# Performance work log

Measured on AMD Instinct MI355X. Metric: run time of the kernel, lower is better.

Reference implementation:

```python
import jax, jax.numpy as jnp
import numpy as np

B, F, D, K, H, W = 8, 16, 256, 3, 64, 64

def setup_inputs() -> dict:
    key = jax.random.key(0)
    k1, k2, k3, k4 = jax.random.split(key, 4)
    return {
        "x": jax.random.normal(k1, (B, D, H, W), dtype=jnp.float32),
        "bank_request": jax.random.normal(k2, (B, F), dtype=jnp.float32),
        "style": jax.random.normal(k3, (B, 1, D, 1, 1), dtype=jnp.float32),
        "bank_weight": jax.random.normal(k4, (F, D, D, K, K), dtype=jnp.float32),
    }

def reference(x, bank_request, style, bank_weight):
    # softmax-weighted filter bank sum -> per-sample kernel (b, o, i, kh, kw)
    w = jax.nn.softmax(bank_request, axis=1)                      # (b, f)
    kernel = jnp.einsum('bf,foihw->boihw', w, bank_weight)
    # style modulation
    kernel = kernel * (1.0 + style)
    # L2 demodulation over (i, kh, kw)
    norm = jax.lax.rsqrt(jnp.sum(kernel * kernel, axis=(2, 3, 4), keepdims=True) + 1e-8)
    kernel = kernel * norm
    # per-sample conv2d, stride 1, SAME padding (odd symmetric kernel)
    def conv_one(xi, ki):
        return jax.lax.conv_general_dilated(
            xi[None], ki, window_strides=(1, 1), padding='SAME',
            dimension_numbers=('NCHW', 'OIHW', 'NCHW'))[0]
    return jax.vmap(conv_one)(x, kernel)
```

## Files before the change

kernel.cpp:

```cpp
#include <hip/hip_runtime.h>
#include <hip/hip_bf16.h>
#include <math.h>

#define BB 8
#define FF 16
#define DD 256
#define HH 64
#define WW 64

typedef short bf16x8 __attribute__((ext_vector_type(8)));
typedef float f32x4 __attribute__((ext_vector_type(4)));

__device__ inline ushort f2bf(float f) {
    union { float f; unsigned u; } v; v.f = f;
    unsigned r = v.u + 0x7FFFu + ((v.u >> 16) & 1u);
    return (ushort)(r >> 16);
}

__global__ __launch_bounds__(256) void cast_x(
    const float* __restrict__ x,
    ushort* __restrict__ xb)
{
    __shared__ ushort ls[64][258];
    const int r = blockIdx.x, b = blockIdx.y, t = threadIdx.x;

    const int c4 = (t & 15) * 4;
    const int ig = t >> 4;
#pragma unroll
    for (int j = 0; j < 16; ++j) {
        const int i = ig * 16 + j;
        const float4 xv = *reinterpret_cast<const float4*>(
            x + (((size_t)(b * DD + i) * HH) + r) * WW + c4);
        ls[c4 + 0][i] = f2bf(xv.x);
        ls[c4 + 1][i] = f2bf(xv.y);
        ls[c4 + 2][i] = f2bf(xv.z);
        ls[c4 + 3][i] = f2bf(xv.w);
    }
    __syncthreads();

    const int i2 = t & 127;
    const int ch = t >> 7;
#pragma unroll
    for (int cl = 0; cl < 32; ++cl) {
        const int c = ch * 32 + cl;
        const unsigned u = (unsigned)ls[c][2 * i2] | ((unsigned)ls[c][2 * i2 + 1] << 16);
        *reinterpret_cast<unsigned*>(xb + (((size_t)(b * HH + r) * WW) + c) * DD + 2 * i2) = u;
    }
}

__global__ __launch_bounds__(256) void prep_filter(
    const float* __restrict__ bank_request,
    const float* __restrict__ style,
    const float* __restrict__ bank_weight,
    ushort* __restrict__ Ak)
{
    const int o = blockIdx.x;
    const int i = threadIdx.x;

    __shared__ float wsm[BB][FF];
    __shared__ float red[4][BB];
    __shared__ float nrm[BB];

    if (i < BB) {
        float v[FF];
        float m = -1e30f;
#pragma unroll
        for (int f = 0; f < FF; ++f) {
            v[f] = bank_request[i * FF + f];
            m = fmaxf(m, v[f]);
        }
        float s = 0.f;
#pragma unroll
        for (int f = 0; f < FF; ++f) { v[f] = __expf(v[f] - m); s += v[f]; }
        const float inv = 1.0f / s;
#pragma unroll
        for (int f = 0; f < FF; ++f) wsm[i][f] = v[f] * inv;
    }
    __syncthreads();

    float acc9[BB][9];
#pragma unroll
    for (int b = 0; b < BB; ++b)
#pragma unroll
        for (int j = 0; j < 9; ++j) acc9[b][j] = 0.f;

    float pre[2][9];
#pragma unroll
    for (int s = 0; s < 2; ++s) {
        const float* p = bank_weight + ((size_t)(s * DD + o) * DD + i) * 9;
#pragma unroll
        for (int j = 0; j < 9; ++j) pre[s][j] = p[j];
    }
#pragma unroll
    for (int f = 0; f < FF; ++f) {
        const int sl = f & 1;
        float cur[9];
#pragma unroll
        for (int j = 0; j < 9; ++j) cur[j] = pre[sl][j];
        if (f + 2 < FF) {
            const float* p = bank_weight + ((size_t)((f + 2) * DD + o) * DD + i) * 9;
#pragma unroll
            for (int j = 0; j < 9; ++j) pre[sl][j] = p[j];
        }
#pragma unroll
        for (int b = 0; b < BB; ++b) {
            const float wf = wsm[b][f];
#pragma unroll
            for (int j = 0; j < 9; ++j) acc9[b][j] = fmaf(wf, cur[j], acc9[b][j]);
        }
    }

    float ss[BB];
#pragma unroll
    for (int b = 0; b < BB; ++b) {
        const float sm = 1.0f + style[b * DD + i];
        float t = 0.f;
#pragma unroll
        for (int j = 0; j < 9; ++j) {
            acc9[b][j] *= sm;
            t = fmaf(acc9[b][j], acc9[b][j], t);
        }
        ss[b] = t;
    }

    const int wave = i >> 6, lane = i & 63;
#pragma unroll
    for (int b = 0; b < BB; ++b) {
        float tv = ss[b];
#pragma unroll
        for (int off = 32; off > 0; off >>= 1) tv += __shfl_down(tv, off, 64);
        if (lane == 0) red[wave][b] = tv;
    }
    __syncthreads();
    if (i < BB)
        nrm[i] = rsqrtf(red[0][i] + red[1][i] + red[2][i] + red[3][i] + 1e-8f);
    __syncthreads();

    const int ib = i >> 3, e = i & 7;
#pragma unroll
    for (int b = 0; b < BB; ++b) {
        const float nb = nrm[b];
#pragma unroll
        for (int j = 0; j < 9; ++j) {
            const size_t idx = ((((size_t)(b * 9 + j) * 32 + ib) * DD) + o) * 8 + e;
            Ak[idx] = f2bf(acc9[b][j] * nb);
        }
    }
}

#define XROWS 4
#define XCELLS 66
#define XCELLB 80
#define XBUF (XROWS * XCELLS * XCELLB)

__global__ __launch_bounds__(512, 4) void conv_mfma(
    const ushort* __restrict__ xb,
    const ushort* __restrict__ Ak,
    float* __restrict__ out)
{
    __shared__ __align__(16) char xs[2 * XBUF];

    const int wg = blockIdx.x;
    const int xcd = wg & 7;
    const int rem = wg >> 3;
    const int rg = rem & 31;
    const int Ghi = rem >> 5;
    const int G = xcd + 8 * Ghi;
    const int ot = G & 1, b = G >> 1;

    const int r0 = rg * 2, o0 = ot * 128;
    const int t = threadIdx.x;
    const int w = t >> 6, l = t & 63;
    const int wm = w & 3;
    const int wn = w >> 2;
    const int lo = l & 15, lhi = l >> 4;

    const ushort* sg_ptr[3];
    int sg_lds[3];
    bool sg_ok[3];
#pragma unroll
    for (int s = 0; s < 3; ++s) {
        const int idx = t + s * 512;
        const bool active = (s < 2) || (t < 32);
        const int row = idx / (XCELLS * 4);
        const int rem2 = idx - row * (XCELLS * 4);
        const int cell = rem2 >> 2;
        const int q = rem2 & 3;
        const int gr = r0 - 1 + row;
        const int gc = cell - 1;
        sg_ok[s] = active && ((unsigned)gr < 64u) && ((unsigned)gc < 64u);
        sg_ptr[s] = xb + (((size_t)(b * HH + (gr & 63)) * WW) + (gc & 63)) * DD + q * 8;
        sg_lds[s] = (row * XCELLS + cell) * XCELLB + q * 16;
    }
    const bool sg_act2 = (t < 32);

    f32x4 acc[2][4];
#pragma unroll
    for (int a = 0; a < 2; ++a)
#pragma unroll
        for (int c = 0; c < 4; ++c)
#pragma unroll
            for (int j = 0; j < 4; ++j) acc[a][c][j] = 0.f;

    const int obase = o0 + wm * 32 + lo;
    const int bLane = lo * XCELLB + lhi * 16;

    bf16x8 vr[3];
    bf16x8 aF[3][2], bF[2][4];

#define LDA(tp, sl, aB)  do {                                                  \
        const ushort* ap_ = (aB) + (size_t)(tp) * 65536;                       \
        aF[sl][0] = *reinterpret_cast<const bf16x8*>(ap_);                     \
        aF[sl][1] = *reinterpret_cast<const bf16x8*>(ap_ + 128);               \
    } while (0)

#define LDB(tp, sl, bufc)  do {                                                \
        const int dr_ = (tp) / 3, dc_ = (tp) % 3;                              \
        const char* bb_ = (bufc) + ((wn + dr_) * XCELLS + dc_) * XCELLB;       \
        bF[sl][0] = *reinterpret_cast<const bf16x8*>(bb_);                     \
        bF[sl][1] = *reinterpret_cast<const bf16x8*>(bb_ + 16 * XCELLB);       \
        bF[sl][2] = *reinterpret_cast<const bf16x8*>(bb_ + 32 * XCELLB);       \
        bF[sl][3] = *reinterpret_cast<const bf16x8*>(bb_ + 48 * XCELLB);       \
    } while (0)

#pragma unroll
    for (int s = 0; s < 3; ++s) {
        if (s < 2 || sg_act2) {
            bf16x8 v = {0, 0, 0, 0, 0, 0, 0, 0};
            if (sg_ok[s]) v = *reinterpret_cast<const bf16x8*>(sg_ptr[s]);
            *reinterpret_cast<bf16x8*>(xs + sg_lds[s]) = v;
        }
    }
    __syncthreads();

    for (int kc = 0; kc < 8; ++kc) {
        const int cur = kc & 1;

        if (kc < 7) {
            const int ioff = (kc + 1) * 32;
#pragma unroll
            for (int s = 0; s < 3; ++s) {
                bf16x8 v = {0, 0, 0, 0, 0, 0, 0, 0};
                if (sg_ok[s]) v = *reinterpret_cast<const bf16x8*>(sg_ptr[s] + ioff);
                vr[s] = v;
            }
        }

        const char* bufc = xs + cur * XBUF + bLane;
        const int ib = kc * 4 + lhi;
        const ushort* aBase = Ak + (((size_t)b * 9 * 32 + ib) * DD + obase) * 8;

        LDA(0, 0, aBase);
        LDA(1, 1, aBase);
        LDB(0, 0, bufc);
#pragma unroll
        for (int tap = 0; tap < 9; ++tap) {
            const int as = tap % 3;
            if (tap + 2 <= 8) LDA(tap + 2, (tap + 2) % 3, aBase);
            if (tap < 8) LDB(tap + 1, (tap + 1) & 1, bufc);
            const int bs = tap & 1;
            __builtin_amdgcn_s_setprio(1);
#pragma unroll
            for (int fm = 0; fm < 2; ++fm)
#pragma unroll
                for (int fn = 0; fn < 4; ++fn)
                    acc[fm][fn] = __builtin_amdgcn_mfma_f32_16x16x32_bf16(
                        aF[as][fm], bF[bs][fn], acc[fm][fn], 0, 0, 0);
            __builtin_amdgcn_s_setprio(0);
        }

        if (kc < 7) {
            char* dstb = xs + (cur ^ 1) * XBUF;
#pragma unroll
            for (int s = 0; s < 3; ++s)
                if (s < 2 || sg_act2)
                    *reinterpret_cast<bf16x8*>(dstb + sg_lds[s]) = vr[s];
        }
        __syncthreads();
    }
#undef LDA
#undef LDB

    const int r_out = r0 + wn;
#pragma unroll
    for (int fm = 0; fm < 2; ++fm) {
#pragma unroll
        for (int fn = 0; fn < 4; ++fn) {
            const int oo = o0 + wm * 32 + fm * 16 + lhi * 4;
            const int cc = fn * 16 + lo;
            float* op = out + (((size_t)(b * DD + oo) * HH) + r_out) * WW + cc;
#pragma unroll
            for (int j = 0; j < 4; ++j) op[(size_t)j * HH * WW] = acc[fm][fn][j];
        }
    }
}

extern "C" void kernel_launch(void* const* d_in, const int* in_sizes, int n_in,
                              void* d_out, int out_size, void* d_ws, size_t ws_size,
                              hipStream_t stream) {
    const float* x            = (const float*)d_in[0];
    const float* bank_request = (const float*)d_in[1];
    const float* style        = (const float*)d_in[2];
    const float* bank_weight  = (const float*)d_in[3];
    float* out = (float*)d_out;

    ushort* Ak = (ushort*)d_ws;
    ushort* xb = Ak + (size_t)8 * 9 * 32 * 256 * 8;

    cast_x<<<dim3(HH, BB), 256, 0, stream>>>(x, xb);
    prep_filter<<<dim3(DD), 256, 0, stream>>>(bank_request, style, bank_weight, Ak);
    conv_mfma<<<dim3(512), 512, 0, stream>>>(xb, Ak, out);
}
```

Baseline: 68.26 us.

## Switch conv to 32x32x16 MFMA with 256-thread blocks and 64x64 wave tiles

Replaces the 16x16x32 bf16 MFMA tiling with 32x32x16 MFMAs, splitting each 32-channel K chunk into two 16-wide substeps. Each workgroup now uses 4 waves instead of 8, each covering a 64x64 output tile, so each wave issues fewer fragment loads per MFMA. The staging loop and the epilogue index mapping are reworked for the new thread count and accumulator layout. Fewer waves per block could reduce latency hiding, and more accumulator registers per wave may lower occupancy.

```diff
diff --git a/kernel.cpp b/kernel.cpp
--- a/kernel.cpp
+++ b/kernel.cpp
@@ -9,7 +9,7 @@
 #define WW 64
 
 typedef short bf16x8 __attribute__((ext_vector_type(8)));
-typedef float f32x4 __attribute__((ext_vector_type(4)));
+typedef float f32x16 __attribute__((ext_vector_type(16)));
 
 __device__ inline ushort f2bf(float f) {
     union { float f; unsigned u; } v; v.f = f;
@@ -153,7 +153,7 @@
 #define XCELLB 80
 #define XBUF (XROWS * XCELLS * XCELLB)
 
-__global__ __launch_bounds__(512, 4) void conv_mfma(
+__global__ __launch_bounds__(256, 2) void conv_mfma(
     const ushort* __restrict__ xb,
     const ushort* __restrict__ Ak,
     float* __restrict__ out)
@@ -171,61 +171,62 @@
     const int r0 = rg * 2, o0 = ot * 128;
     const int t = threadIdx.x;
     const int w = t >> 6, l = t & 63;
-    const int wm = w & 3;
-    const int wn = w >> 2;
-    const int lo = l & 15, lhi = l >> 4;
-
-    const ushort* sg_ptr[3];
-    int sg_lds[3];
-    bool sg_ok[3];
-#pragma unroll
-    for (int s = 0; s < 3; ++s) {
-        const int idx = t + s * 512;
-        const bool active = (s < 2) || (t < 32);
+    const int wm = w >> 1;
+    const int wn = w & 1;
+    const int l31 = l & 31, lhi = l >> 5;
+
+    const ushort* sg_ptr[5];
+    int sg_lds[5];
+    bool sg_ok[5];
+    bool sg_act[5];
+#pragma unroll
+    for (int s = 0; s < 5; ++s) {
+        const int idx = t + s * 256;
+        sg_act[s] = (s < 4) || (t < 32);
         const int row = idx / (XCELLS * 4);
         const int rem2 = idx - row * (XCELLS * 4);
         const int cell = rem2 >> 2;
         const int q = rem2 & 3;
         const int gr = r0 - 1 + row;
         const int gc = cell - 1;
-        sg_ok[s] = active && ((unsigned)gr < 64u) && ((unsigned)gc < 64u);
+        sg_ok[s] = sg_act[s] && ((unsigned)gr < 64u) && ((unsigned)gc < 64u);
         sg_ptr[s] = xb + (((size_t)(b * HH + (gr & 63)) * WW) + (gc & 63)) * DD + q * 8;
         sg_lds[s] = (row * XCELLS + cell) * XCELLB + q * 16;
     }
-    const bool sg_act2 = (t < 32);
-
-    f32x4 acc[2][4];
+
+    f32x16 acc[2][2];
 #pragma unroll
     for (int a = 0; a < 2; ++a)
 #pragma unroll
-        for (int c = 0; c < 4; ++c)
-#pragma unroll
-            for (int j = 0; j < 4; ++j) acc[a][c][j] = 0.f;
-
-    const int obase = o0 + wm * 32 + lo;
-    const int bLane = lo * XCELLB + lhi * 16;
-
-    bf16x8 vr[3];
-    bf16x8 aF[3][2], bF[2][4];
-
-#define LDA(tp, sl, aB)  do {                                                  \
-        const ushort* ap_ = (aB) + (size_t)(tp) * 65536;                       \
+        for (int c = 0; c < 2; ++c)
+#pragma unroll
+            for (int j = 0; j < 16; ++j) acc[a][c][j] = 0.f;
+
+    const int obase = o0 + wm * 64 + l31;
+    const int bLane = l31 * XCELLB + lhi * 16;
+
+    bf16x8 vr[5];
+    bf16x8 aF[3][2], bF[2][2];
+
+#define LDA(stp, sl, aB)  do {                                                 \
+        const int tp_ = (stp) >> 1, ks_ = (stp) & 1;                           \
+        const ushort* ap_ = (aB) + tp_ * 65536 + ks_ * 4096;                   \
         aF[sl][0] = *reinterpret_cast<const bf16x8*>(ap_);                     \
-        aF[sl][1] = *reinterpret_cast<const bf16x8*>(ap_ + 128);               \
+        aF[sl][1] = *reinterpret_cast<const bf16x8*>(ap_ + 256);               \
     } while (0)
 
-#define LDB(tp, sl, bufc)  do {                                                \
-        const int dr_ = (tp) / 3, dc_ = (tp) % 3;                              \
-        const char* bb_ = (bufc) + ((wn + dr_) * XCELLS + dc_) * XCELLB;       \
+#define LDB(stp, sl, bufc)  do {                                               \
+        const int tp_ = (stp) >> 1, ks_ = (stp) & 1;                           \
+        const int dr_ = tp_ / 3, dc_ = tp_ % 3;                                \
+        const char* bb_ = (bufc) + ((wn + dr_) * XCELLS + dc_) * XCELLB        \
+                          + ks_ * 32;                                          \
         bF[sl][0] = *reinterpret_cast<const bf16x8*>(bb_);                     \
-        bF[sl][1] = *reinterpret_cast<const bf16x8*>(bb_ + 16 * XCELLB);       \
-        bF[sl][2] = *reinterpret_cast<const bf16x8*>(bb_ + 32 * XCELLB);       \
-        bF[sl][3] = *reinterpret_cast<const bf16x8*>(bb_ + 48 * XCELLB);       \
+        bF[sl][1] = *reinterpret_cast<const bf16x8*>(bb_ + 32 * XCELLB);       \
     } while (0)
 
 #pragma unroll
-    for (int s = 0; s < 3; ++s) {
-        if (s < 2 || sg_act2) {
+    for (int s = 0; s < 5; ++s) {
+        if (sg_act[s]) {
             bf16x8 v = {0, 0, 0, 0, 0, 0, 0, 0};
             if (sg_ok[s]) v = *reinterpret_cast<const bf16x8*>(sg_ptr[s]);
             *reinterpret_cast<bf16x8*>(xs + sg_lds[s]) = v;
@@ -239,7 +240,7 @@
         if (kc < 7) {
             const int ioff = (kc + 1) * 32;
 #pragma unroll
-            for (int s = 0; s < 3; ++s) {
+            for (int s = 0; s < 5; ++s) {
                 bf16x8 v = {0, 0, 0, 0, 0, 0, 0, 0};
                 if (sg_ok[s]) v = *reinterpret_cast<const bf16x8*>(sg_ptr[s] + ioff);
                 vr[s] = v;
@@ -247,24 +248,28 @@
         }
 
         const char* bufc = xs + cur * XBUF + bLane;
-        const int ib = kc * 4 + lhi;
-        const ushort* aBase = Ak + (((size_t)b * 9 * 32 + ib) * DD + obase) * 8;
-
-        LDA(0, 0, aBase);
-        LDA(1, 1, aBase);
+        const ushort* aBase =
+            Ak + ((((size_t)b * 9 * 32) + kc * 4 + lhi * 1) * DD + obase) * 8
+               + 0;
+        const ushort* aLane =
+            Ak + ((((size_t)b * 9 * 32) + kc * 4 + lhi) * DD + obase) * 8;
+        (void)aBase;
+
+        LDA(0, 0, aLane);
+        LDA(1, 1, aLane);
         LDB(0, 0, bufc);
 #pragma unroll
-        for (int tap = 0; tap < 9; ++tap) {
-            const int as = tap % 3;
-            if (tap + 2 <= 8) LDA(tap + 2, (tap + 2) % 3, aBase);
-            if (tap < 8) LDB(tap + 1, (tap + 1) & 1, bufc);
-            const int bs = tap & 1;
+        for (int stp = 0; stp < 18; ++stp) {
+            const int as = stp % 3;
+            if (stp + 2 < 18) LDA(stp + 2, (stp + 2) % 3, aLane);
+            if (stp + 1 < 18) LDB(stp + 1, (stp + 1) & 1, bufc);
+            const int bs = stp & 1;
             __builtin_amdgcn_s_setprio(1);
 #pragma unroll
             for (int fm = 0; fm < 2; ++fm)
 #pragma unroll
-                for (int fn = 0; fn < 4; ++fn)
-                    acc[fm][fn] = __builtin_amdgcn_mfma_f32_16x16x32_bf16(
+                for (int fn = 0; fn < 2; ++fn)
+                    acc[fm][fn] = __builtin_amdgcn_mfma_f32_32x32x16_bf16(
                         aF[as][fm], bF[bs][fn], acc[fm][fn], 0, 0, 0);
             __builtin_amdgcn_s_setprio(0);
         }
@@ -272,9 +277,8 @@
         if (kc < 7) {
             char* dstb = xs + (cur ^ 1) * XBUF;
 #pragma unroll
-            for (int s = 0; s < 3; ++s)
-                if (s < 2 || sg_act2)
-                    *reinterpret_cast<bf16x8*>(dstb + sg_lds[s]) = vr[s];
+            for (int s = 0; s < 5; ++s)
+                if (sg_act[s]) *reinterpret_cast<bf16x8*>(dstb + sg_lds[s]) = vr[s];
         }
         __syncthreads();
     }
@@ -285,12 +289,15 @@
 #pragma unroll
     for (int fm = 0; fm < 2; ++fm) {
 #pragma unroll
-        for (int fn = 0; fn < 4; ++fn) {
-            const int oo = o0 + wm * 32 + fm * 16 + lhi * 4;
-            const int cc = fn * 16 + lo;
-            float* op = out + (((size_t)(b * DD + oo) * HH) + r_out) * WW + cc;
-#pragma unroll
-            for (int j = 0; j < 4; ++j) op[(size_t)j * HH * WW] = acc[fm][fn][j];
+        for (int fn = 0; fn < 2; ++fn) {
+            const int cc = fn * 32 + l31;
+#pragma unroll
+            for (int reg = 0; reg < 16; ++reg) {
+                const int oo = o0 + wm * 64 + fm * 32
+                             + (reg & 3) + 8 * (reg >> 2) + 4 * lhi;
+                out[(((size_t)(b * DD + oo) * HH) + r_out) * WW + cc] =
+                    acc[fm][fn][reg];
+            }
         }
     }
 }
@@ -309,5 +316,5 @@
 
     cast_x<<<dim3(HH, BB), 256, 0, stream>>>(x, xb);
     prep_filter<<<dim3(DD), 256, 0, stream>>>(bank_request, style, bank_weight, Ak);
-    conv_mfma<<<dim3(512), 512, 0, stream>>>(xb, Ak, out);
-}
+    conv_mfma<<<dim3(512), 256, 0, stream>>>(xb, Ak, out);
+}
```

After: 71.58 us. 4.9% more time.

## Fuse prep kernels and retile conv to one output row per block

Applied to the files above, without the earlier changes.

The x-cast and filter-prep kernels are merged into one launch, with block ranges selecting the role, so one kernel launch and its tail are removed. The conv kernel drops from 512-thread blocks covering two output rows to 256-thread blocks covering one row, doubling the grid and shrinking the LDS halo buffer from 4 to 3 rows. The global prefetch of the next channel chunk moves to mid-tap, behind a sched barrier, to overlap with MFMA work. Per-output halo reuse drops (3 input rows per output row instead of 2), trading extra LDS fill traffic for more blocks and better occupancy.

```diff
diff --git a/kernel.cpp b/kernel.cpp
--- a/kernel.cpp
+++ b/kernel.cpp
@@ -17,50 +17,52 @@
     return (ushort)(r >> 16);
 }
 
-__global__ __launch_bounds__(256) void cast_x(
+__global__ __launch_bounds__(256) void prep_fused(
     const float* __restrict__ x,
-    ushort* __restrict__ xb)
-{
-    __shared__ ushort ls[64][258];
-    const int r = blockIdx.x, b = blockIdx.y, t = threadIdx.x;
-
-    const int c4 = (t & 15) * 4;
-    const int ig = t >> 4;
-#pragma unroll
-    for (int j = 0; j < 16; ++j) {
-        const int i = ig * 16 + j;
-        const float4 xv = *reinterpret_cast<const float4*>(
-            x + (((size_t)(b * DD + i) * HH) + r) * WW + c4);
-        ls[c4 + 0][i] = f2bf(xv.x);
-        ls[c4 + 1][i] = f2bf(xv.y);
-        ls[c4 + 2][i] = f2bf(xv.z);
-        ls[c4 + 3][i] = f2bf(xv.w);
-    }
-    __syncthreads();
-
-    const int i2 = t & 127;
-    const int ch = t >> 7;
-#pragma unroll
-    for (int cl = 0; cl < 32; ++cl) {
-        const int c = ch * 32 + cl;
-        const unsigned u = (unsigned)ls[c][2 * i2] | ((unsigned)ls[c][2 * i2 + 1] << 16);
-        *reinterpret_cast<unsigned*>(xb + (((size_t)(b * HH + r) * WW) + c) * DD + 2 * i2) = u;
-    }
-}
-
-__global__ __launch_bounds__(256) void prep_filter(
     const float* __restrict__ bank_request,
     const float* __restrict__ style,
     const float* __restrict__ bank_weight,
+    ushort* __restrict__ xb,
     ushort* __restrict__ Ak)
 {
-    const int o = blockIdx.x;
-    const int i = threadIdx.x;
-
+    __shared__ ushort ls[64][258];
     __shared__ float wsm[BB][FF];
     __shared__ float red[4][BB];
     __shared__ float nrm[BB];
 
+    const int t = threadIdx.x;
+
+    if (blockIdx.x < 512) {
+        const int r = blockIdx.x & 63, b = blockIdx.x >> 6;
+
+        const int c4 = (t & 15) * 4;
+        const int ig = t >> 4;
+#pragma unroll
+        for (int j = 0; j < 16; ++j) {
+            const int i = ig * 16 + j;
+            const float4 xv = *reinterpret_cast<const float4*>(
+                x + (((size_t)(b * DD + i) * HH) + r) * WW + c4);
+            ls[c4 + 0][i] = f2bf(xv.x);
+            ls[c4 + 1][i] = f2bf(xv.y);
+            ls[c4 + 2][i] = f2bf(xv.z);
+            ls[c4 + 3][i] = f2bf(xv.w);
+        }
+        __syncthreads();
+
+        const int i2 = t & 127;
+        const int ch = t >> 7;
+#pragma unroll
+        for (int cl = 0; cl < 32; ++cl) {
+            const int c = ch * 32 + cl;
+            const unsigned u = (unsigned)ls[c][2 * i2] | ((unsigned)ls[c][2 * i2 + 1] << 16);
+            *reinterpret_cast<unsigned*>(xb + (((size_t)(b * HH + r) * WW) + c) * DD + 2 * i2) = u;
+        }
+        return;
+    }
+
+    const int o = blockIdx.x - 512;
+    const int i = t;
+
     if (i < BB) {
         float v[FF];
         float m = -1e30f;
@@ -114,13 +116,13 @@
 #pragma unroll
     for (int b = 0; b < BB; ++b) {
         const float sm = 1.0f + style[b * DD + i];
-        float t = 0.f;
+        float tv = 0.f;
 #pragma unroll
         for (int j = 0; j < 9; ++j) {
             acc9[b][j] *= sm;
-            t = fmaf(acc9[b][j], acc9[b][j], t);
-        }
-        ss[b] = t;
+            tv = fmaf(acc9[b][j], acc9[b][j], tv);
+        }
+        ss[b] = tv;
     }
 
     const int wave = i >> 6, lane = i & 63;
@@ -148,12 +150,12 @@
     }
 }
 
-#define XROWS 4
+#define XROWS 3
 #define XCELLS 66
 #define XCELLB 80
 #define XBUF (XROWS * XCELLS * XCELLB)
 
-__global__ __launch_bounds__(512, 4) void conv_mfma(
+__global__ __launch_bounds__(256, 4) void conv_mfma(
     const ushort* __restrict__ xb,
     const ushort* __restrict__ Ak,
     float* __restrict__ out)
@@ -163,36 +165,34 @@
     const int wg = blockIdx.x;
     const int xcd = wg & 7;
     const int rem = wg >> 3;
-    const int rg = rem & 31;
-    const int Ghi = rem >> 5;
+    const int r0 = rem & 63;
+    const int Ghi = rem >> 6;
     const int G = xcd + 8 * Ghi;
     const int ot = G & 1, b = G >> 1;
 
-    const int r0 = rg * 2, o0 = ot * 128;
+    const int o0 = ot * 128;
     const int t = threadIdx.x;
     const int w = t >> 6, l = t & 63;
-    const int wm = w & 3;
-    const int wn = w >> 2;
     const int lo = l & 15, lhi = l >> 4;
 
-    const ushort* sg_ptr[3];
-    int sg_lds[3];
-    bool sg_ok[3];
-#pragma unroll
-    for (int s = 0; s < 3; ++s) {
-        const int idx = t + s * 512;
-        const bool active = (s < 2) || (t < 32);
+    const ushort* sg_ptr[4];
+    int sg_lds[4];
+    bool sg_ok[4];
+    bool sg_act[4];
+#pragma unroll
+    for (int s = 0; s < 4; ++s) {
+        const int idx = t + s * 256;
+        sg_act[s] = (s < 3) || (t < 792 - 768);
         const int row = idx / (XCELLS * 4);
         const int rem2 = idx - row * (XCELLS * 4);
         const int cell = rem2 >> 2;
         const int q = rem2 & 3;
         const int gr = r0 - 1 + row;
         const int gc = cell - 1;
-        sg_ok[s] = active && ((unsigned)gr < 64u) && ((unsigned)gc < 64u);
+        sg_ok[s] = sg_act[s] && ((unsigned)gr < 64u) && ((unsigned)gc < 64u);
         sg_ptr[s] = xb + (((size_t)(b * HH + (gr & 63)) * WW) + (gc & 63)) * DD + q * 8;
         sg_lds[s] = (row * XCELLS + cell) * XCELLB + q * 16;
     }
-    const bool sg_act2 = (t < 32);
 
     f32x4 acc[2][4];
 #pragma unroll
@@ -202,10 +202,10 @@
 #pragma unroll
             for (int j = 0; j < 4; ++j) acc[a][c][j] = 0.f;
 
-    const int obase = o0 + wm * 32 + lo;
+    const int obase = o0 + w * 32 + lo;
     const int bLane = lo * XCELLB + lhi * 16;
 
-    bf16x8 vr[3];
+    bf16x8 vr[4];
     bf16x8 aF[3][2], bF[2][4];
 
 #define LDA(tp, sl, aB)  do {                                                  \
@@ -216,7 +216,7 @@
 
 #define LDB(tp, sl, bufc)  do {                                                \
         const int dr_ = (tp) / 3, dc_ = (tp) % 3;                              \
-        const char* bb_ = (bufc) + ((wn + dr_) * XCELLS + dc_) * XCELLB;       \
+        const char* bb_ = (bufc) + (dr_ * XCELLS + dc_) * XCELLB;              \
         bF[sl][0] = *reinterpret_cast<const bf16x8*>(bb_);                     \
         bF[sl][1] = *reinterpret_cast<const bf16x8*>(bb_ + 16 * XCELLB);       \
         bF[sl][2] = *reinterpret_cast<const bf16x8*>(bb_ + 32 * XCELLB);       \
@@ -224,8 +224,8 @@
     } while (0)
 
 #pragma unroll
-    for (int s = 0; s < 3; ++s) {
-        if (s < 2 || sg_act2) {
+    for (int s = 0; s < 4; ++s) {
+        if (sg_act[s]) {
             bf16x8 v = {0, 0, 0, 0, 0, 0, 0, 0};
             if (sg_ok[s]) v = *reinterpret_cast<const bf16x8*>(sg_ptr[s]);
             *reinterpret_cast<bf16x8*>(xs + sg_lds[s]) = v;
@@ -235,28 +235,18 @@
 
     for (int kc = 0; kc < 8; ++kc) {
         const int cur = kc & 1;
-
-        if (kc < 7) {
-            const int ioff = (kc + 1) * 32;
-#pragma unroll
-            for (int s = 0; s < 3; ++s) {
-                bf16x8 v = {0, 0, 0, 0, 0, 0, 0, 0};
-                if (sg_ok[s]) v = *reinterpret_cast<const bf16x8*>(sg_ptr[s] + ioff);
-                vr[s] = v;
-            }
-        }
-
         const char* bufc = xs + cur * XBUF + bLane;
         const int ib = kc * 4 + lhi;
-        const ushort* aBase = Ak + (((size_t)b * 9 * 32 + ib) * DD + obase) * 8;
-
-        LDA(0, 0, aBase);
-        LDA(1, 1, aBase);
+        const ushort* aLane =
+            Ak + ((((size_t)b * 9 * 32) + ib) * DD + obase) * 8;
+
+        LDA(0, 0, aLane);
+        LDA(1, 1, aLane);
         LDB(0, 0, bufc);
 #pragma unroll
         for (int tap = 0; tap < 9; ++tap) {
             const int as = tap % 3;
-            if (tap + 2 <= 8) LDA(tap + 2, (tap + 2) % 3, aBase);
+            if (tap + 2 <= 8) LDA(tap + 2, (tap + 2) % 3, aLane);
             if (tap < 8) LDB(tap + 1, (tap + 1) & 1, bufc);
             const int bs = tap & 1;
             __builtin_amdgcn_s_setprio(1);
@@ -267,28 +257,37 @@
                     acc[fm][fn] = __builtin_amdgcn_mfma_f32_16x16x32_bf16(
                         aF[as][fm], bF[bs][fn], acc[fm][fn], 0, 0, 0);
             __builtin_amdgcn_s_setprio(0);
+
+            if (tap == 4 && kc < 7) {
+                __builtin_amdgcn_sched_barrier(0);
+                const int ioff = (kc + 1) * 32;
+#pragma unroll
+                for (int s = 0; s < 4; ++s) {
+                    bf16x8 v = {0, 0, 0, 0, 0, 0, 0, 0};
+                    if (sg_ok[s]) v = *reinterpret_cast<const bf16x8*>(sg_ptr[s] + ioff);
+                    vr[s] = v;
+                }
+            }
         }
 
         if (kc < 7) {
             char* dstb = xs + (cur ^ 1) * XBUF;
 #pragma unroll
-            for (int s = 0; s < 3; ++s)
-                if (s < 2 || sg_act2)
-                    *reinterpret_cast<bf16x8*>(dstb + sg_lds[s]) = vr[s];
+            for (int s = 0; s < 4; ++s)
+                if (sg_act[s]) *reinterpret_cast<bf16x8*>(dstb + sg_lds[s]) = vr[s];
         }
         __syncthreads();
     }
 #undef LDA
 #undef LDB
 
-    const int r_out = r0 + wn;
 #pragma unroll
     for (int fm = 0; fm < 2; ++fm) {
 #pragma unroll
         for (int fn = 0; fn < 4; ++fn) {
-            const int oo = o0 + wm * 32 + fm * 16 + lhi * 4;
+            const int oo = o0 + w * 32 + fm * 16 + lhi * 4;
             const int cc = fn * 16 + lo;
-            float* op = out + (((size_t)(b * DD + oo) * HH) + r_out) * WW + cc;
+            float* op = out + (((size_t)(b * DD + oo) * HH) + r0) * WW + cc;
 #pragma unroll
             for (int j = 0; j < 4; ++j) op[(size_t)j * HH * WW] = acc[fm][fn][j];
         }
@@ -307,7 +306,6 @@
     ushort* Ak = (ushort*)d_ws;
     ushort* xb = Ak + (size_t)8 * 9 * 32 * 256 * 8;
 
-    cast_x<<<dim3(HH, BB), 256, 0, stream>>>(x, xb);
-    prep_filter<<<dim3(DD), 256, 0, stream>>>(bank_request, style, bank_weight, Ak);
-    conv_mfma<<<dim3(512), 512, 0, stream>>>(xb, Ak, out);
+    prep_fused<<<dim3(768), 256, 0, stream>>>(x, bank_request, style, bank_weight, xb, Ak);
+    conv_mfma<<<dim3(1024), 256, 0, stream>>>(xb, Ak, out);
 }
```

Measured after the change: 71.51 us. +4.8%, slower.
